# Kernel tuning notes

Hardware: AMD Instinct MI355X
Metric: run time of the kernel (lower is better)

Reference implementation:

```python
import jax, jax.numpy as jnp
import numpy as np

B, N, C = 32, 256, 4096
H = 16
HEAD_DIM = C // H  # 256 == N, required by the module's math
SCALE = HEAD_DIM ** -0.5


def setup_inputs() -> dict:
    key = jax.random.key(0)
    ks = jax.random.split(key, 7)
    std = C ** -0.5
    return {
        "x1": jax.random.normal(ks[0], (B, N, C), dtype=jnp.float32),
        "x2": jax.random.normal(ks[1], (B, N, C), dtype=jnp.float32),
        "Wq": jax.random.normal(ks[2], (C, C), dtype=jnp.float32) * std,
        "Wk": jax.random.normal(ks[3], (C, C), dtype=jnp.float32) * std,
        "Wv": jax.random.normal(ks[4], (C, C), dtype=jnp.float32) * std,
        "Wp": jax.random.normal(ks[5], (C, C), dtype=jnp.float32) * std,
        "bp": jnp.zeros((C,), dtype=jnp.float32),
    }


def reference(x1, x2, Wq, Wk, Wv, Wp, bp):
    b, n, c = x1.shape
    h, hd = H, HEAD_DIM
    # QKV projections (qkv_bias=False); q pre-scaled as in source
    q = (x1 @ Wq.T) * SCALE
    k = x2 @ Wk.T
    v = x2 @ Wv.T
    split = lambda t: t.reshape(b, n, h, hd).transpose(0, 2, 1, 3)  # b h n hd
    q, k, v = split(q), split(k), split(v)
    # channel-wise attention: q^T @ k over the token axis -> [b, h, hd, hd]
    attn = jax.nn.softmax(jnp.einsum("bhni,bhnj->bhij", q, k), axis=-1)
    # attn @ v: inner dim of attn (hd) contracts with token axis of v (n == hd)
    out = jnp.einsum("bhin,bhnc->bhic", attn, v)  # [b, h, hd, hd]
    out = out.transpose(0, 2, 1, 3).reshape(b, n, c)
    x = out @ Wp.T + bp
    return (x, attn)
```

## Files before the change

kernel.cpp:

```cpp
#include <hip/hip_runtime.h>

typedef __attribute__((ext_vector_type(4))) float f32x4;
typedef __attribute__((ext_vector_type(8))) short short8;
typedef __attribute__((ext_vector_type(4))) unsigned short ushort4v;

__device__ __forceinline__ unsigned short rne_bf16(float f) {
  unsigned int u = __builtin_bit_cast(unsigned int, f);
  u += 0x7FFFu + ((u >> 16) & 1u);
  return (unsigned short)(u >> 16);
}

__device__ __forceinline__ void async16(void* lds, const void* g) {
  __builtin_amdgcn_global_load_lds(
      (const __attribute__((address_space(1))) void*)g,
      (__attribute__((address_space(3))) void*)lds, 16, 0, 0);
}

__device__ __forceinline__ f32x4 mfma16(short8 a, short8 b, f32x4 c) {
  return __builtin_amdgcn_mfma_f32_16x16x32_bf16(a, b, c, 0, 0, 0);
}

__global__ __launch_bounds__(256) void cast_k(const float* __restrict__ in,
                                              unsigned short* __restrict__ out,
                                              int n4) {
  int stride = gridDim.x * 256;
  for (int i = blockIdx.x * 256 + threadIdx.x; i < n4; i += stride) {
    float4 v = ((const float4*)in)[i];
    ushort4v o = {rne_bf16(v.x), rne_bf16(v.y), rne_bf16(v.z), rne_bf16(v.w)};
    ((ushort4v*)out)[i] = o;
  }
}

template <int MODE>
__global__ __launch_bounds__(512, 2) void gemm256(const unsigned short* __restrict__ A,
                                                  const unsigned short* __restrict__ B,
                                                  float* __restrict__ outF,
                                                  unsigned short* __restrict__ outB,
                                                  const float* __restrict__ bias,
                                                  int K, int lda, int ldb,
                                                  float scale, int gx) {
  __shared__ unsigned short lds[65536];
  const int tid = threadIdx.x;
  const int lane = tid & 63;
  const int wid = tid >> 6;
  const int wm = wid >> 2;
  const int wn = wid & 3;
  int lin = blockIdx.x;
  lin = (lin & 7) * (gridDim.x >> 3) + (lin >> 3);
  const int bx = lin % gx;
  const int by = lin / gx;
  const int m0 = by * 256, n0 = bx * 256;
  const int NT = K >> 6;

  const int gsw8 = (((tid & 3) ^ ((tid >> 3) & 3))) * 8;
  const unsigned short* gA = A + (size_t)(m0 + (tid >> 2)) * lda + gsw8;
  const unsigned short* gB = B + (size_t)(n0 + (tid >> 2)) * ldb + gsw8;
  const size_t astep = (size_t)128 * lda;
  const size_t bstep = (size_t)128 * ldb;
  unsigned short* ld0 = &lds[tid * 8];

#define STG(Q) do { \
    const int kt_ = ((Q) >> 1) * 64 + ((Q) & 1) * 32; \
    const int off_ = (((Q) >> 1) & 1) * 32768 + ((Q) & 1) * 8192; \
    const unsigned short* sA_ = gA + kt_; \
    unsigned short* dA_ = ld0 + off_; \
    async16(dA_, sA_); async16(dA_ + 4096, sA_ + astep); \
    const unsigned short* sB_ = gB + kt_; \
    unsigned short* dB_ = ld0 + 16384 + off_; \
    async16(dB_, sB_); async16(dB_ + 4096, sB_ + bstep); } while (0)

  const int rl = lane & 15;
  const int ch = (lane >> 4) ^ ((rl >> 1) & 3);
  const int aidx = wm * 4096 + rl * 32 + ch * 8;
  const int bidx = 16384 + wn * 2048 + rl * 32 + ch * 8;

  short8 af[8], bf0[4], bf1[4];
#define READ_A(base) do { \
    _Pragma("unroll") \
    for (int r_ = 0; r_ < 8; ++r_) af[r_] = *(const short8*)&lds[(base) + aidx + r_ * 512]; \
  } while (0)
#define READ_B(base, dst) do { \
    _Pragma("unroll") \
    for (int s_ = 0; s_ < 4; ++s_) dst[s_] = *(const short8*)&lds[(base) + bidx + s_ * 512]; \
  } while (0)

  f32x4 acc[8][4];
#pragma unroll
  for (int r = 0; r < 8; ++r)
#pragma unroll
    for (int s = 0; s < 4; ++s) acc[r][s] = (f32x4){0.f, 0.f, 0.f, 0.f};

#define MFMA32(bfX) do { \
    __builtin_amdgcn_s_setprio(1); \
    _Pragma("unroll") \
    for (int r_ = 0; r_ < 8; ++r_) \
      _Pragma("unroll") \
      for (int s_ = 0; s_ < 4; ++s_) acc[r_][s_] = mfma16(af[r_], bfX[s_], acc[r_][s_]); \
    __builtin_amdgcn_s_setprio(0); \
  } while (0)

  STG(0); STG(1); STG(2);
  asm volatile("s_waitcnt vmcnt(4)" ::: "memory");
  __builtin_amdgcn_s_barrier();
  READ_B(0, bf0);

  for (int t = 0; t < NT; ++t) {
    const int bb = (t & 1) * 32768;
    READ_A(bb);
    READ_B(bb + 8192, bf1);
    if (t + 1 < NT) STG(2 * t + 3);
    __builtin_amdgcn_sched_barrier(0);
    MFMA32(bf0);
    if (t + 1 < NT) asm volatile("s_waitcnt vmcnt(4)" ::: "memory");
    else            asm volatile("s_waitcnt vmcnt(0)" ::: "memory");
    __builtin_amdgcn_s_barrier();
    READ_A(bb + 8192);
    if (t + 1 < NT) {
      READ_B(((t + 1) & 1) * 32768, bf0);
      if (t + 2 < NT) STG(2 * t + 4);
    }
    __builtin_amdgcn_sched_barrier(0);
    MFMA32(bf1);
    if (t + 1 < NT) {
      if (t + 2 < NT) asm volatile("s_waitcnt vmcnt(4)" ::: "memory");
      else            asm volatile("s_waitcnt vmcnt(0)" ::: "memory");
      __builtin_amdgcn_s_barrier();
    }
  }
#undef STG
#undef READ_A
#undef READ_B
#undef MFMA32

  const int fcol = lane & 15;
  const int frow = (lane >> 4) * 4;
#pragma unroll
  for (int r = 0; r < 8; ++r) {
#pragma unroll
    for (int s = 0; s < 4; ++s) {
      f32x4 v = acc[r][s];
      const int m = m0 + wm * 128 + r * 16 + frow;
      const int n = n0 + wn * 64 + s * 16 + fcol;
      if (MODE == 0) {
        ushort4v p;
#pragma unroll
        for (int j = 0; j < 4; ++j) p[j] = rne_bf16(v[j] * scale);
        size_t d = ((size_t)((m >> 8) * 16 + (n >> 8))) * 65536 +
                   (size_t)(n & 255) * 256 + (m & 255);
        *(ushort4v*)&outB[d] = p;
      } else {
        float bv = bias[n];
#pragma unroll
        for (int j = 0; j < 4; ++j) outF[(size_t)(m + j) * 4096 + n] = v[j] + bv;
      }
    }
  }
}

__global__ __launch_bounds__(256) void attn_fused(const unsigned short* __restrict__ Qt,
                                                  const unsigned short* __restrict__ Kt,
                                                  const unsigned short* __restrict__ Vt,
                                                  float* __restrict__ outA,
                                                  unsigned short* __restrict__ outXb) {
  __shared__ unsigned short sh[34560];
  const int tid = threadIdx.x;
  const int lane = tid & 63;
  const int wid = tid >> 6;
  const int z = blockIdx.y;
  const int m0 = blockIdx.x * 64;
  const int wm = wid >> 1;
  const int wn = wid & 1;
  const int fcol = lane & 15;
  const int kslot = (lane >> 4) * 8;
  const int frow = (lane >> 4) * 4;

  const unsigned short* Qh = Qt + (size_t)z * 65536;
  const unsigned short* Kh = Kt + (size_t)z * 65536;
  const unsigned short* Vh = Vt + (size_t)z * 65536;
  float* redM = (float*)&sh[33536];
  float* redS = redM + 128;

  f32x4 acc[2][8];
#pragma unroll
  for (int r = 0; r < 2; ++r)
#pragma unroll
    for (int s = 0; s < 8; ++s) acc[r][s] = (f32x4){0.f, 0.f, 0.f, 0.f};

  {
    const int arow = tid >> 2;
    const int acol = (tid & 3) * 8;
    const unsigned short* gQ = Qh + (size_t)(m0 + arow) * 256 + acol;
    const unsigned short* gK = Kh + (size_t)arow * 256 + acol;
    unsigned short* lA = &sh[tid * 8];
    unsigned short* lB = &sh[2048 + tid * 8];

    for (int kt = 0; kt < 256; kt += 32) {
      __syncthreads();
      async16(lA, gQ + kt);
      async16(lB, gK + kt);
      async16(lB + 2048, gK + (size_t)64 * 256 + kt);
      async16(lB + 4096, gK + (size_t)128 * 256 + kt);
      async16(lB + 6144, gK + (size_t)192 * 256 + kt);
      __syncthreads();

      short8 a[2], b[8];
#pragma unroll
      for (int r = 0; r < 2; ++r)
        a[r] = *(const short8*)&sh[(wm * 32 + r * 16 + fcol) * 32 + kslot];
#pragma unroll
      for (int s = 0; s < 8; ++s)
        b[s] = *(const short8*)&sh[2048 + (wn * 128 + s * 16 + fcol) * 32 + kslot];
#pragma unroll
      for (int r = 0; r < 2; ++r)
#pragma unroll
        for (int s = 0; s < 8; ++s)
          acc[r][s] = mfma16(a[r], b[s], acc[r][s]);
    }
  }
  __syncthreads();

#pragma unroll
  for (int r = 0; r < 2; ++r) {
#pragma unroll
    for (int j = 0; j < 4; ++j) {
      float m = acc[r][0][j];
#pragma unroll
      for (int s = 1; s < 8; ++s) m = fmaxf(m, acc[r][s][j]);
#pragma unroll
      for (int off = 1; off < 16; off <<= 1) m = fmaxf(m, __shfl_xor(m, off, 64));
      if (fcol == 0) redM[(wm * 32 + r * 16 + frow + j) * 2 + wn] = m;
    }
  }
  __syncthreads();
#pragma unroll
  for (int r = 0; r < 2; ++r) {
#pragma unroll
    for (int j = 0; j < 4; ++j) {
      const int rl = wm * 32 + r * 16 + frow + j;
      const float m = fmaxf(redM[rl * 2 + 0], redM[rl * 2 + 1]);
      float sum = 0.f;
#pragma unroll
      for (int s = 0; s < 8; ++s) {
        float e = __expf(acc[r][s][j] - m);
        acc[r][s][j] = e;
        sum += e;
      }
#pragma unroll
      for (int off = 1; off < 16; off <<= 1) sum += __shfl_xor(sum, off, 64);
      if (fcol == 0) redS[rl * 2 + wn] = sum;
    }
  }
  __syncthreads();
#pragma unroll
  for (int r = 0; r < 2; ++r) {
#pragma unroll
    for (int j = 0; j < 4; ++j) {
      const int rl = wm * 32 + r * 16 + frow + j;
      const float inv = 1.0f / (redS[rl * 2 + 0] + redS[rl * 2 + 1]);
      const size_t rowo = (size_t)z * 65536 + (size_t)(m0 + rl) * 256;
#pragma unroll
      for (int s = 0; s < 8; ++s) {
        const int col = wn * 128 + s * 16 + fcol;
        const float p = acc[r][s][j] * inv;
        outA[rowo + col] = p;
        sh[16384 + rl * 268 + col] = rne_bf16(p);
      }
    }
  }
  __syncthreads();

  const unsigned short* gV = Vh + (size_t)(tid >> 2) * 256 + (tid & 3) * 8;
#define STGV(kt, vb) do { \
    _Pragma("unroll") \
    for (int k_ = 0; k_ < 4; ++k_) \
      async16(&sh[(vb) + tid * 8 + k_ * 2048], \
              gV + (size_t)k_ * 64 * 256 + (kt) * 32); } while (0)

  STGV(0, 0); STGV(1, 8192);
  asm volatile("s_waitcnt vmcnt(4)" ::: "memory");
  __builtin_amdgcn_s_barrier();

  f32x4 acc2[2][8];
#pragma unroll
  for (int r = 0; r < 2; ++r)
#pragma unroll
    for (int s = 0; s < 8; ++s) acc2[r][s] = (f32x4){0.f, 0.f, 0.f, 0.f};

  for (int kt = 0; kt < 8; ++kt) {
    const int vb = (kt & 1) * 8192;
    short8 a2[2], b2[8];
#pragma unroll
    for (int r = 0; r < 2; ++r)
      a2[r] = *(const short8*)&sh[16384 + (wm * 32 + r * 16 + fcol) * 268 + kt * 32 + kslot];
#pragma unroll
    for (int s = 0; s < 8; ++s)
      b2[s] = *(const short8*)&sh[vb + (wn * 128 + s * 16 + fcol) * 32 + kslot];
#pragma unroll
    for (int r = 0; r < 2; ++r)
#pragma unroll
      for (int s = 0; s < 8; ++s)
        acc2[r][s] = mfma16(a2[r], b2[s], acc2[r][s]);
    __builtin_amdgcn_s_barrier();
    if (kt + 2 < 8) {
      STGV(kt + 2, vb);
      asm volatile("s_waitcnt vmcnt(4)" ::: "memory");
    } else {
      asm volatile("s_waitcnt vmcnt(0)" ::: "memory");
    }
    __builtin_amdgcn_s_barrier();
  }
#undef STGV

#pragma unroll
  for (int r = 0; r < 2; ++r) {
#pragma unroll
    for (int s = 0; s < 8; ++s) {
      f32x4 v = acc2[r][s];
      const int i0 = m0 + wm * 32 + r * 16 + frow;
      const int c = wn * 128 + s * 16 + fcol;
#pragma unroll
      for (int j = 0; j < 4; ++j) {
        size_t d = ((size_t)((z >> 4) * 256 + i0 + j)) * 4096 + (z & 15) * 256 + c;
        outXb[d] = rne_bf16(v[j]);
      }
    }
  }
}

extern "C" void kernel_launch(void* const* d_in, const int* in_sizes, int n_in,
                              void* d_out, int out_size, void* d_ws, size_t ws_size,
                              hipStream_t stream) {
  const float* x1 = (const float*)d_in[0];
  const float* x2 = (const float*)d_in[1];
  const float* Wq = (const float*)d_in[2];
  const float* Wk = (const float*)d_in[3];
  const float* Wv = (const float*)d_in[4];
  const float* Wp = (const float*)d_in[5];
  const float* bp = (const float*)d_in[6];

  float* outX = (float*)d_out;
  float* outA = outX + (size_t)33554432;

  unsigned short* Qt  = (unsigned short*)d_ws;
  unsigned short* Kt  = Qt + 33554432;
  unsigned short* Vt  = Kt + 33554432;
  unsigned short* x1b = Vt + 33554432;
  unsigned short* x2b = x1b + 33554432;
  unsigned short* Wb  = x2b + 33554432;

  const float SCALE = 0.0625f;

  cast_k<<<2048, 256, 0, stream>>>(x1, x1b, 8388608);
  cast_k<<<2048, 256, 0, stream>>>(x2, x2b, 8388608);

  cast_k<<<2048, 256, 0, stream>>>(Wq, Wb, 4194304);
  gemm256<0><<<512, 512, 0, stream>>>(x1b, Wb, nullptr, Qt, nullptr,
                                      4096, 4096, 4096, SCALE, 16);
  cast_k<<<2048, 256, 0, stream>>>(Wk, Wb, 4194304);
  gemm256<0><<<512, 512, 0, stream>>>(x2b, Wb, nullptr, Kt, nullptr,
                                      4096, 4096, 4096, 1.0f, 16);
  cast_k<<<2048, 256, 0, stream>>>(Wv, Wb, 4194304);
  gemm256<0><<<512, 512, 0, stream>>>(x2b, Wb, nullptr, Vt, nullptr,
                                      4096, 4096, 4096, 1.0f, 16);

  attn_fused<<<dim3(4, 512), 256, 0, stream>>>(Qt, Kt, Vt, outA, x2b);

  cast_k<<<2048, 256, 0, stream>>>(Wp, Wb, 4194304);
  gemm256<3><<<512, 512, 0, stream>>>(x2b, Wb, outX, nullptr, bp,
                                      4096, 4096, 4096, 1.0f, 16);
}
```

Before: 1.264 ms.

## Split GEMM main loop into four half-tile phases with finer LDS prefetch

```diff
diff --git a/kernel.cpp b/kernel.cpp
--- a/kernel.cpp
+++ b/kernel.cpp
@@ -74,14 +74,16 @@
   const int aidx = wm * 4096 + rl * 32 + ch * 8;
   const int bidx = 16384 + wn * 2048 + rl * 32 + ch * 8;
 
-  short8 af[8], bf0[4], bf1[4];
-#define READ_A(base) do { \
+  short8 afA[4], afB[4], bfA[4], bfB[4];
+#define READ_AF(dst, base, hf) do { \
     _Pragma("unroll") \
-    for (int r_ = 0; r_ < 8; ++r_) af[r_] = *(const short8*)&lds[(base) + aidx + r_ * 512]; \
+    for (int r_ = 0; r_ < 4; ++r_) \
+      dst[r_] = *(const short8*)&lds[(base) + aidx + ((hf) * 4 + r_) * 512]; \
   } while (0)
-#define READ_B(base, dst) do { \
+#define READ_BF(dst, base) do { \
     _Pragma("unroll") \
-    for (int s_ = 0; s_ < 4; ++s_) dst[s_] = *(const short8*)&lds[(base) + bidx + s_ * 512]; \
+    for (int s_ = 0; s_ < 4; ++s_) \
+      dst[s_] = *(const short8*)&lds[(base) + bidx + s_ * 512]; \
   } while (0)
 
   f32x4 acc[8][4];
@@ -90,47 +92,64 @@
 #pragma unroll
     for (int s = 0; s < 4; ++s) acc[r][s] = (f32x4){0.f, 0.f, 0.f, 0.f};
 
-#define MFMA32(bfX) do { \
+#define MFMA16(afX, bfX, o) do { \
     __builtin_amdgcn_s_setprio(1); \
     _Pragma("unroll") \
-    for (int r_ = 0; r_ < 8; ++r_) \
+    for (int r_ = 0; r_ < 4; ++r_) \
       _Pragma("unroll") \
-      for (int s_ = 0; s_ < 4; ++s_) acc[r_][s_] = mfma16(af[r_], bfX[s_], acc[r_][s_]); \
+      for (int s_ = 0; s_ < 4; ++s_) \
+        acc[(o) + r_][s_] = mfma16(afX[r_], bfX[s_], acc[(o) + r_][s_]); \
     __builtin_amdgcn_s_setprio(0); \
   } while (0)
 
+#define GATE4() asm volatile("s_waitcnt vmcnt(4)" ::: "memory")
+#define GATE0() asm volatile("s_waitcnt vmcnt(0)" ::: "memory")
+
   STG(0); STG(1); STG(2);
-  asm volatile("s_waitcnt vmcnt(4)" ::: "memory");
+  asm volatile("s_waitcnt vmcnt(8)" ::: "memory");
   __builtin_amdgcn_s_barrier();
-  READ_B(0, bf0);
+  READ_AF(afA, 0, 0);
+  READ_BF(bfA, 0);
 
   for (int t = 0; t < NT; ++t) {
-    const int bb = (t & 1) * 32768;
-    READ_A(bb);
-    READ_B(bb + 8192, bf1);
-    if (t + 1 < NT) STG(2 * t + 3);
-    __builtin_amdgcn_sched_barrier(0);
-    MFMA32(bf0);
-    if (t + 1 < NT) asm volatile("s_waitcnt vmcnt(4)" ::: "memory");
-    else            asm volatile("s_waitcnt vmcnt(0)" ::: "memory");
-    __builtin_amdgcn_s_barrier();
-    READ_A(bb + 8192);
-    if (t + 1 < NT) {
-      READ_B(((t + 1) & 1) * 32768, bf0);
-      if (t + 2 < NT) STG(2 * t + 4);
-    }
-    __builtin_amdgcn_sched_barrier(0);
-    MFMA32(bf1);
-    if (t + 1 < NT) {
-      if (t + 2 < NT) asm volatile("s_waitcnt vmcnt(4)" ::: "memory");
-      else            asm volatile("s_waitcnt vmcnt(0)" ::: "memory");
-      __builtin_amdgcn_s_barrier();
-    }
+    const int rb0 = (t & 1) * 32768;
+    const int rb1 = rb0 + 8192;
+    const int rbn = ((t + 1) & 1) * 32768;
+    const bool s1 = (t + 1) < NT;
+    const bool s2 = (t + 2) < NT;
+
+    if (s1) STG(2 * t + 3);
+    READ_AF(afB, rb0, 1);
+    MFMA16(afA, bfA, 0);
+    if (s1) GATE4(); else GATE0();
+    __builtin_amdgcn_s_barrier();
+
+    READ_AF(afA, rb1, 0);
+    READ_BF(bfB, rb1);
+    MFMA16(afB, bfA, 4);
+    if (s1) GATE4(); else GATE0();
+    __builtin_amdgcn_s_barrier();
+
+    if (s2) STG(2 * t + 4);
+    READ_AF(afB, rb1, 1);
+    MFMA16(afA, bfB, 0);
+    if (s2) GATE4(); else GATE0();
+    __builtin_amdgcn_s_barrier();
+
+    if (s1) {
+      READ_AF(afA, rbn, 0);
+      READ_BF(bfA, rbn);
+    }
+    MFMA16(afB, bfB, 4);
+    if (s2) GATE4(); else GATE0();
+    __builtin_amdgcn_s_barrier();
   }
 #undef STG
-#undef READ_A
-#undef READ_B
-#undef MFMA32
+#undef READ_AF
+#undef READ_BF
+#undef MFMA16
+#undef GATE4
+#undef GATE0
 
   const int fcol = lane & 15;
   const int frow = (lane >> 4) * 4;
```

New measurement: 1.292 ms. +2.2%, slower.

## Fuse fp32-to-bf16 weight cast into GEMM B-tile loading

Applied to the files above, without the earlier changes.

```diff
diff --git a/kernel.cpp b/kernel.cpp
--- a/kernel.cpp
+++ b/kernel.cpp
@@ -2,6 +2,7 @@
 
 typedef __attribute__((ext_vector_type(4))) float f32x4;
 typedef __attribute__((ext_vector_type(8))) short short8;
+typedef __attribute__((ext_vector_type(8))) unsigned short ushort8v;
 typedef __attribute__((ext_vector_type(4))) unsigned short ushort4v;
 
 __device__ __forceinline__ unsigned short rne_bf16(float f) {
@@ -33,7 +34,7 @@
 
 template <int MODE>
 __global__ __launch_bounds__(512, 2) void gemm256(const unsigned short* __restrict__ A,
-                                                  const unsigned short* __restrict__ B,
+                                                  const float* __restrict__ Bw,
                                                   float* __restrict__ outF,
                                                   unsigned short* __restrict__ outB,
                                                   const float* __restrict__ bias,
@@ -54,20 +55,34 @@
 
   const int gsw8 = (((tid & 3) ^ ((tid >> 3) & 3))) * 8;
   const unsigned short* gA = A + (size_t)(m0 + (tid >> 2)) * lda + gsw8;
-  const unsigned short* gB = B + (size_t)(n0 + (tid >> 2)) * ldb + gsw8;
+  const float* gW = Bw + (size_t)(n0 + (tid >> 2)) * ldb + gsw8;
   const size_t astep = (size_t)128 * lda;
-  const size_t bstep = (size_t)128 * ldb;
+  const size_t wstep = (size_t)128 * ldb;
   unsigned short* ld0 = &lds[tid * 8];
 
-#define STG(Q) do { \
-    const int kt_ = ((Q) >> 1) * 64 + ((Q) & 1) * 32; \
-    const int off_ = (((Q) >> 1) & 1) * 32768 + ((Q) & 1) * 8192; \
-    const unsigned short* sA_ = gA + kt_; \
-    unsigned short* dA_ = ld0 + off_; \
-    async16(dA_, sA_); async16(dA_ + 4096, sA_ + astep); \
-    const unsigned short* sB_ = gB + kt_; \
-    unsigned short* dB_ = ld0 + 16384 + off_; \
-    async16(dB_, sB_); async16(dB_ + 4096, sB_ + bstep); } while (0)
+#define ROFF(Q) ((((Q) >> 1) & 1) * 32768 + ((Q) & 1) * 8192)
+#define RKT(Q) (((Q) >> 1) * 64 + ((Q) & 1) * 32)
+
+#define STG_A(Q) do { \
+    const unsigned short* sA_ = gA + RKT(Q); \
+    unsigned short* dA_ = ld0 + ROFF(Q); \
+    async16(dA_, sA_); async16(dA_ + 4096, sA_ + astep); } while (0)
+
+  float4 wl0, wl1, wl2, wl3;
+#define WLOAD(Q) do { \
+    const float* sW_ = gW + RKT(Q); \
+    wl0 = *(const float4*)(sW_); \
+    wl1 = *(const float4*)(sW_ + 4); \
+    wl2 = *(const float4*)(sW_ + wstep); \
+    wl3 = *(const float4*)(sW_ + wstep + 4); } while (0)
+#define WSTORE(Q) do { \
+    unsigned short* dB_ = ld0 + 16384 + ROFF(Q); \
+    ushort8v p0_ = {rne_bf16(wl0.x), rne_bf16(wl0.y), rne_bf16(wl0.z), rne_bf16(wl0.w), \
+                    rne_bf16(wl1.x), rne_bf16(wl1.y), rne_bf16(wl1.z), rne_bf16(wl1.w)}; \
+    ushort8v p1_ = {rne_bf16(wl2.x), rne_bf16(wl2.y), rne_bf16(wl2.z), rne_bf16(wl2.w), \
+                    rne_bf16(wl3.x), rne_bf16(wl3.y), rne_bf16(wl3.z), rne_bf16(wl3.w)}; \
+    *(ushort8v*)dB_ = p0_; \
+    *(ushort8v*)(dB_ + 4096) = p1_; } while (0)
 
   const int rl = lane & 15;
   const int ch = (lane >> 4) ^ ((rl >> 1) & 3);
@@ -99,38 +114,55 @@
     __builtin_amdgcn_s_setprio(0); \
   } while (0)
 
-  STG(0); STG(1); STG(2);
-  asm volatile("s_waitcnt vmcnt(4)" ::: "memory");
+#define LGKM0() asm volatile("s_waitcnt lgkmcnt(0)" ::: "memory")
+
+  WLOAD(0); WSTORE(0);
+  WLOAD(1); WSTORE(1);
+  WLOAD(2);
+  STG_A(0); STG_A(1); STG_A(2);
+  asm volatile("s_waitcnt vmcnt(2)" ::: "memory");
+  LGKM0();
   __builtin_amdgcn_s_barrier();
   READ_B(0, bf0);
 
   for (int t = 0; t < NT; ++t) {
-    const int bb = (t & 1) * 32768;
-    READ_A(bb);
-    READ_B(bb + 8192, bf1);
-    if (t + 1 < NT) STG(2 * t + 3);
+    const int rb0 = (t & 1) * 32768;
+    const int rb1 = rb0 + 8192;
+    const int rbn = ((t + 1) & 1) * 32768;
+    const bool s1 = (t + 1) < NT;
+    const bool s2 = (t + 2) < NT;
+
+    if (s1) WSTORE(2 * t + 2);
+    if (s1) { WLOAD(2 * t + 3); STG_A(2 * t + 3); }
+    READ_A(rb0);
+    READ_B(rb1, bf1);
     __builtin_amdgcn_sched_barrier(0);
     MFMA32(bf0);
-    if (t + 1 < NT) asm volatile("s_waitcnt vmcnt(4)" ::: "memory");
-    else            asm volatile("s_waitcnt vmcnt(0)" ::: "memory");
+    if (s1) asm volatile("s_waitcnt vmcnt(6)" ::: "memory");
+    else    asm volatile("s_waitcnt vmcnt(0)" ::: "memory");
+    LGKM0();
     __builtin_amdgcn_s_barrier();
-    READ_A(bb + 8192);
-    if (t + 1 < NT) {
-      READ_B(((t + 1) & 1) * 32768, bf0);
-      if (t + 2 < NT) STG(2 * t + 4);
-    }
+
+    if (s1) WSTORE(2 * t + 3);
+    if (s2) { WLOAD(2 * t + 4); STG_A(2 * t + 4); }
+    READ_A(rb1);
+    if (s1) READ_B(rbn, bf0);
     __builtin_amdgcn_sched_barrier(0);
     MFMA32(bf1);
-    if (t + 1 < NT) {
-      if (t + 2 < NT) asm volatile("s_waitcnt vmcnt(4)" ::: "memory");
-      else            asm volatile("s_waitcnt vmcnt(0)" ::: "memory");
-      __builtin_amdgcn_s_barrier();
-    }
-  }
-#undef STG
+    if (s2)      asm volatile("s_waitcnt vmcnt(6)" ::: "memory");
+    else         asm volatile("s_waitcnt vmcnt(0)" ::: "memory");
+    LGKM0();
+    __builtin_amdgcn_s_barrier();
+  }
+#undef STG_A
+#undef WLOAD
+#undef WSTORE
 #undef READ_A
 #undef READ_B
 #undef MFMA32
+#undef LGKM0
+#undef ROFF
+#undef RKT
 
   const int fcol = lane & 15;
   const int frow = (lane >> 4) * 4;
@@ -346,26 +378,21 @@
   unsigned short* Vt  = Kt + 33554432;
   unsigned short* x1b = Vt + 33554432;
   unsigned short* x2b = x1b + 33554432;
-  unsigned short* Wb  = x2b + 33554432;
 
   const float SCALE = 0.0625f;
 
   cast_k<<<2048, 256, 0, stream>>>(x1, x1b, 8388608);
   cast_k<<<2048, 256, 0, stream>>>(x2, x2b, 8388608);
 
-  cast_k<<<2048, 256, 0, stream>>>(Wq, Wb, 4194304);
-  gemm256<0><<<512, 512, 0, stream>>>(x1b, Wb, nullptr, Qt, nullptr,
+  gemm256<0><<<512, 512, 0, stream>>>(x1b, Wq, nullptr, Qt, nullptr,
                                       4096, 4096, 4096, SCALE, 16);
-  cast_k<<<2048, 256, 0, stream>>>(Wk, Wb, 4194304);
-  gemm256<0><<<512, 512, 0, stream>>>(x2b, Wb, nullptr, Kt, nullptr,
+  gemm256<0><<<512, 512, 0, stream>>>(x2b, Wk, nullptr, Kt, nullptr,
                                       4096, 4096, 4096, 1.0f, 16);
-  cast_k<<<2048, 256, 0, stream>>>(Wv, Wb, 4194304);
-  gemm256<0><<<512, 512, 0, stream>>>(x2b, Wb, nullptr, Vt, nullptr,
+  gemm256<0><<<512, 512, 0, stream>>>(x2b, Wv, nullptr, Vt, nullptr,
                                       4096, 4096, 4096, 1.0f, 16);
 
   attn_fused<<<dim3(4, 512), 256, 0, stream>>>(Qt, Kt, Vt, outA, x2b);
 
-  cast_k<<<2048, 256, 0, stream>>>(Wp, Wb, 4194304);
-  gemm256<3><<<512, 512, 0, stream>>>(x2b, Wb, outX, nullptr, bp,
+  gemm256<3><<<512, 512, 0, stream>>>(x2b, Wp, outX, nullptr, bp,
                                       4096, 4096, 4096, 1.0f, 16);
 }
```

Measured after the change: 1.451 ms. 1.15x slower.

## Fuse all input casts into one kernel and batch QKV GEMMs via grid z

Applied to the files above, without the earlier changes.

```diff
diff --git a/kernel.cpp b/kernel.cpp
--- a/kernel.cpp
+++ b/kernel.cpp
@@ -31,20 +31,57 @@
   }
 }
 
+__global__ __launch_bounds__(256) void cast_all(const float* __restrict__ x1,
+                                                const float* __restrict__ x2,
+                                                const float* __restrict__ Wq,
+                                                const float* __restrict__ Wk,
+                                                const float* __restrict__ Wv,
+                                                const float* __restrict__ Wp,
+                                                unsigned short* __restrict__ x1b,
+                                                unsigned short* __restrict__ x2b,
+                                                unsigned short* __restrict__ Wb4) {
+  const int stride = gridDim.x * 256;
+  for (int i = blockIdx.x * 256 + threadIdx.x; i < 33554432; i += stride) {
+    const float* src;
+    unsigned short* dst;
+    int off;
+    if (i < 8388608) {
+      src = x1; dst = x1b; off = i;
+    } else if (i < 16777216) {
+      src = x2; dst = x2b; off = i - 8388608;
+    } else {
+      const int w = (i - 16777216) >> 22;
+      off = (i - 16777216) & 4194303;
+      src = (w == 0) ? Wq : (w == 1) ? Wk : (w == 2) ? Wv : Wp;
+      dst = Wb4 + (size_t)w * 16777216;
+    }
+    float4 v = ((const float4*)src)[off];
+    ushort4v o = {rne_bf16(v.x), rne_bf16(v.y), rne_bf16(v.z), rne_bf16(v.w)};
+    ((ushort4v*)dst)[off] = o;
+  }
+}
+
 template <int MODE>
-__global__ __launch_bounds__(512, 2) void gemm256(const unsigned short* __restrict__ A,
-                                                  const unsigned short* __restrict__ B,
+__global__ __launch_bounds__(512, 2) void gemm256(const unsigned short* __restrict__ A1,
+                                                  const unsigned short* __restrict__ A2,
+                                                  const unsigned short* __restrict__ Bb,
+                                                  size_t wstride,
                                                   float* __restrict__ outF,
-                                                  unsigned short* __restrict__ outB,
+                                                  unsigned short* __restrict__ outB0,
                                                   const float* __restrict__ bias,
                                                   int K, int lda, int ldb,
-                                                  float scale, int gx) {
+                                                  float scale0, float scale1, int gx) {
   __shared__ unsigned short lds[65536];
   const int tid = threadIdx.x;
   const int lane = tid & 63;
   const int wid = tid >> 6;
   const int wm = wid >> 2;
   const int wn = wid & 3;
+  const int z = blockIdx.z;
+  const unsigned short* A = z ? A2 : A1;
+  const unsigned short* B = Bb + (size_t)z * wstride;
+  unsigned short* outB = (MODE == 0) ? outB0 + (size_t)z * 33554432 : outB0;
+  const float scale = z ? scale1 : scale0;
   int lin = blockIdx.x;
   lin = (lin & 7) * (gridDim.x >> 3) + (lin >> 3);
   const int bx = lin % gx;
@@ -346,26 +383,36 @@
   unsigned short* Vt  = Kt + 33554432;
   unsigned short* x1b = Vt + 33554432;
   unsigned short* x2b = x1b + 33554432;
-  unsigned short* Wb  = x2b + 33554432;
 
   const float SCALE = 0.0625f;
-
-  cast_k<<<2048, 256, 0, stream>>>(x1, x1b, 8388608);
-  cast_k<<<2048, 256, 0, stream>>>(x2, x2b, 8388608);
-
-  cast_k<<<2048, 256, 0, stream>>>(Wq, Wb, 4194304);
-  gemm256<0><<<512, 512, 0, stream>>>(x1b, Wb, nullptr, Qt, nullptr,
-                                      4096, 4096, 4096, SCALE, 16);
-  cast_k<<<2048, 256, 0, stream>>>(Wk, Wb, 4194304);
-  gemm256<0><<<512, 512, 0, stream>>>(x2b, Wb, nullptr, Kt, nullptr,
-                                      4096, 4096, 4096, 1.0f, 16);
-  cast_k<<<2048, 256, 0, stream>>>(Wv, Wb, 4194304);
-  gemm256<0><<<512, 512, 0, stream>>>(x2b, Wb, nullptr, Vt, nullptr,
-                                      4096, 4096, 4096, 1.0f, 16);
-
-  attn_fused<<<dim3(4, 512), 256, 0, stream>>>(Qt, Kt, Vt, outA, x2b);
-
-  cast_k<<<2048, 256, 0, stream>>>(Wp, Wb, 4194304);
-  gemm256<3><<<512, 512, 0, stream>>>(x2b, Wb, outX, nullptr, bp,
-                                      4096, 4096, 4096, 1.0f, 16);
-}
+  const bool big = ws_size >= 469762048ULL;
+
+  if (big) {
+    unsigned short* Wb4 = x2b + 33554432;
+    cast_all<<<2048, 256, 0, stream>>>(x1, x2, Wq, Wk, Wv, Wp, x1b, x2b, Wb4);
+    gemm256<0><<<dim3(512, 1, 3), 512, 0, stream>>>(
+        x1b, x2b, Wb4, (size_t)16777216, nullptr, Qt, nullptr,
+        4096, 4096, 4096, SCALE, 1.0f, 16);
+    attn_fused<<<dim3(4, 512), 256, 0, stream>>>(Qt, Kt, Vt, outA, x2b);
+    gemm256<3><<<dim3(512, 1, 1), 512, 0, stream>>>(
+        x2b, x2b, Wb4 + (size_t)50331648, 0, outX, nullptr, bp,
+        4096, 4096, 4096, 1.0f, 1.0f, 16);
+  } else {
+    unsigned short* Wb = x2b + 33554432;
+    cast_k<<<2048, 256, 0, stream>>>(x1, x1b, 8388608);
+    cast_k<<<2048, 256, 0, stream>>>(x2, x2b, 8388608);
+    cast_k<<<2048, 256, 0, stream>>>(Wq, Wb, 4194304);
+    gemm256<0><<<dim3(512, 1, 1), 512, 0, stream>>>(
+        x1b, x1b, Wb, 0, nullptr, Qt, nullptr, 4096, 4096, 4096, SCALE, SCALE, 16);
+    cast_k<<<2048, 256, 0, stream>>>(Wk, Wb, 4194304);
+    gemm256<0><<<dim3(512, 1, 1), 512, 0, stream>>>(
+        x2b, x2b, Wb, 0, nullptr, Kt, nullptr, 4096, 4096, 4096, 1.0f, 1.0f, 16);
+    cast_k<<<2048, 256, 0, stream>>>(Wv, Wb, 4194304);
+    gemm256<0><<<dim3(512, 1, 1), 512, 0, stream>>>(
+        x2b, x2b, Wb, 0, nullptr, Vt, nullptr, 4096, 4096, 4096, 1.0f, 1.0f, 16);
+    attn_fused<<<dim3(4, 512), 256, 0, stream>>>(Qt, Kt, Vt, outA, x2b);
+    cast_k<<<2048, 256, 0, stream>>>(Wp, Wb, 4194304);
+    gemm256<3><<<dim3(512, 1, 1), 512, 0, stream>>>(
+        x2b, x2b, Wb, 0, outX, nullptr, bp, 4096, 4096, 4096, 1.0f, 1.0f, 16);
+  }
+}
```

Result: no change. 1.265 ms (median of 2 runs) (+0.1%).
